# Performance work log

Hardware: AMD Instinct MI355X
Metric: run time of the kernel (lower is better)

## Reference

```python
import jax, jax.numpy as jnp
import numpy as np

DEPTH = 4      # truncation depth of the signature
DIM = 8        # path channels
PATH_LEN = 16384
STREAM = True


def _restricted_exp(z, depth):
    # exp(z) in truncated tensor algebra: level k term = z^{\otimes k}/k!, flattened to [d**k]
    terms = [z]
    for k in range(2, depth + 1):
        terms.append((terms[-1][:, None] * z[None, :]).reshape(-1) / k)
    return tuple(terms)


def _chen_mult(a, b, depth):
    # Truncated tensor-algebra product (Chen's relation); a_0 = b_0 = 1 implicit.
    # c_k = a_k + b_k + sum_{i=1}^{k-1} a_i \otimes b_{k-i}
    c = []
    for k in range(depth):
        t = a[k] + b[k]
        for i in range(k):
            t = t + (a[i][:, None] * b[k - 1 - i][None, :]).reshape(-1)
        c.append(t)
    return tuple(c)


def setup_inputs() -> dict:
    key = jax.random.key(0)
    path = jax.random.normal(key, (PATH_LEN, DIM), dtype=jnp.float32)
    return {"path": path}


def reference(path):
    depth = DEPTH
    d = path.shape[-1]
    inc = path[1:] - path[:-1]                                # [N-1, d] increments
    exps = jax.vmap(lambda z: _restricted_exp(z, depth))(inc)  # tuple of [N-1, d**k]
    init = tuple(jnp.zeros((d ** (k + 1),), dtype=path.dtype) for k in range(depth))

    def step(carry, x):
        new = _chen_mult(carry, x, depth)
        return new, (new if STREAM else None)

    last, ys = jax.lax.scan(step, init, exps)
    if STREAM:
        # flatten: concat levels -> [N-1, d + d^2 + ... + d^depth]
        return jnp.concatenate([y for y in ys], axis=-1)
    return jnp.concatenate(last, axis=-1)
```

## Files before the change

### kernel.cpp

```cpp
#include <hip/hip_runtime.h>

#define NPATH 16384
#define DIM   8
#define NINC  (NPATH - 1)
#define SIG   4680
#define L1OFF 0
#define L2OFF 8
#define L3OFF 72
#define L4OFF 584
#define NBLK  256
#define CHUNK 64
#define NGRP  16
#define GSIZE 16
#define C6    0.16666666666666666f


__device__ __forceinline__ void store_sig_reg(float* __restrict__ dst,
                                              const float r4[16], const float r3[2],
                                              float a2s, float a1t, int t) {
  float4* d4 = (float4*)(dst + L4OFF + 16 * t);
  d4[0] = make_float4(r4[0], r4[1], r4[2], r4[3]);
  d4[1] = make_float4(r4[4], r4[5], r4[6], r4[7]);
  d4[2] = make_float4(r4[8], r4[9], r4[10], r4[11]);
  d4[3] = make_float4(r4[12], r4[13], r4[14], r4[15]);
  *(float2*)(dst + L3OFF + 2 * t) = make_float2(r3[0], r3[1]);
  if (t < 64) dst[L2OFF + t] = a2s;
  if (t < 8)  dst[L1OFF + t] = a1t;
}

__device__ __forceinline__ void chen_reg(float r4[16], float r3[2],
                                         float& a1i, float& a2v,
                                         float& a2s, float& a1s, float& a1t,
                                         const float* __restrict__ b, int t) {
  const int i   = t >> 5;
  const int j   = (t >> 2) & 7;
  const int ij  = t >> 2;
  const int c0  = 2 * t;
  const int jk0 = c0 & 63;
  const int k0  = 2 * (t & 3);
  const int i2  = t >> 3;
  const int j2  = t & 7;
  const float4* bv = (const float4*)b;
  float4 B0 = bv[146 + 4 * t], B1 = bv[147 + 4 * t], B2 = bv[148 + 4 * t], B3 = bv[149 + 4 * t];
  float4 Cq0 = bv[18 + 2 * jk0], Cq1 = bv[19 + 2 * jk0], Cq2 = bv[20 + 2 * jk0], Cq3 = bv[21 + 2 * jk0];
  float4 D0 = bv[2 + 2 * k0], D1 = bv[3 + 2 * k0], D2 = bv[4 + 2 * k0], D3 = bv[5 + 2 * k0];
  float4 E0 = bv[0], E1 = bv[1];
  const float2 b3c  = *(const float2*)(b + L3OFF + c0);
  const float2 b2jk = *(const float2*)(b + L2OFF + jk0);
  const float2 b1k  = *(const float2*)(b + L1OFF + k0);
  const float b2ij = b[L2OFF + ij];
  const float b1j  = b[L1OFF + j];
  const float b1i  = b[L1OFF + i];
  float b2t = 0.f, b1j2 = 0.f, b1i2 = 0.f, b1t = 0.f;
  if (t < 64) { b2t = b[L2OFF + t]; b1j2 = b[L1OFF + j2]; b1i2 = b[L1OFF + i2]; }
  if (t < 8)  { b1t = b[L1OFF + t]; }

  const float b4r[16] = {B0.x,B0.y,B0.z,B0.w, B1.x,B1.y,B1.z,B1.w,
                         B2.x,B2.y,B2.z,B2.w, B3.x,B3.y,B3.z,B3.w};
  const float b3r[16] = {Cq0.x,Cq0.y,Cq0.z,Cq0.w, Cq1.x,Cq1.y,Cq1.z,Cq1.w,
                         Cq2.x,Cq2.y,Cq2.z,Cq2.w, Cq3.x,Cq3.y,Cq3.z,Cq3.w};
  const float b2r[16] = {D0.x,D0.y,D0.z,D0.w, D1.x,D1.y,D1.z,D1.w,
                         D2.x,D2.y,D2.z,D2.w, D3.x,D3.y,D3.z,D3.w};
  const float b1r[8]  = {E0.x,E0.y,E0.z,E0.w, E1.x,E1.y,E1.z,E1.w};

#pragma unroll
  for (int l = 0; l < 8; ++l) {
    r4[l]     += b4r[l]     + a1i * b3r[l]     + a2v * b2r[l]     + r3[0] * b1r[l];
    r4[8 + l] += b4r[8 + l] + a1i * b3r[8 + l] + a2v * b2r[8 + l] + r3[1] * b1r[l];
  }
  r3[0] += b3c.x + a1i * b2jk.x + a2v * b1k.x;
  r3[1] += b3c.y + a1i * b2jk.y + a2v * b1k.y;
  const float a1i_old = a1i;
  a2v += b2ij + a1i_old * b1j;
  if (t < 64) { a2s += b2t + a1s * b1j2; a1s += b1i2; }
  a1i = a1i_old + b1i;
  if (t < 8) a1t += b1t;
}

__device__ __forceinline__ void fill_zbuf(float (*zbuf)[8], const float* __restrict__ path,
                                          int base, int t) {
  for (int u = t; u < CHUNK * 8; u += 256) {
    const int s = u >> 3, l = u & 7;
    const int rB = min(base + s + 1, NPATH - 1);
    zbuf[s][l] = path[rB * DIM + l] - path[(base + s) * DIM + l];
  }
}

template <bool STORE>
__device__ __forceinline__ void run_steps(const float (*zbuf)[8],
                                          float* __restrict__ out, int base, int nsteps,
                                          float r4[16], float r3[2],
                                          float& a1i, float& a2v,
                                          float& a2s, float& a1s, float& a1t, int t) {
  const int i  = t >> 5;
  const int j  = (t >> 2) & 7;
  const int k0 = 2 * (t & 3);
  const int i2 = t >> 3;
  const int j2 = t & 7;
  for (int s = 0; s < nsteps; ++s) {
    const float* zs = zbuf[s];
    const float zi = zs[i];
    const float zj = zs[j];
    const float2 zk = *(const float2*)(zs + k0);
    const float4 za = *(const float4*)zs;
    const float4 zb = *(const float4*)(zs + 4);
    const float zn[8] = {za.x, za.y, za.z, za.w, zb.x, zb.y, zb.z, zb.w};
    const float a1zi4 = a1i + 0.25f * zi;
    const float zj6   = C6 * zj;
    const float T0 = r3[0] + a2v * (0.5f * zk.x) + a1zi4 * (zj6 * zk.x);
    const float T1 = r3[1] + a2v * (0.5f * zk.y) + a1zi4 * (zj6 * zk.y);
    const float U  = a2v + (0.5f * a1i + C6 * zi) * zj;
#pragma unroll
    for (int l = 0; l < 8; ++l) {
      r4[l]     += T0 * zn[l];
      r4[8 + l] += T1 * zn[l];
    }
    r3[0] += zk.x * U;
    r3[1] += zk.y * U;
    a2v += (a1i + 0.5f * zi) * zj;
    a1i += zi;
    if (t < 64) {
      const float zi2 = zs[i2], zj2v = zs[j2];
      a2s += (a1s + 0.5f * zi2) * zj2v;
      a1s += zi2;
    }
    if (t < 8) a1t += zs[t];
    if constexpr (STORE) {
      float* dst = out + (size_t)(base + s) * SIG;
      float4* d4 = (float4*)(dst + L4OFF + 16 * t);
      d4[0] = make_float4(r4[0], r4[1], r4[2], r4[3]);
      d4[1] = make_float4(r4[4], r4[5], r4[6], r4[7]);
      d4[2] = make_float4(r4[8], r4[9], r4[10], r4[11]);
      d4[3] = make_float4(r4[12], r4[13], r4[14], r4[15]);
      *(float2*)(dst + L3OFF + 2 * t) = make_float2(r3[0], r3[1]);
      if (t < 64) dst[L2OFF + t] = a2s;
      if (t < 8)  dst[L1OFF + t] = a1t;
    }
  }
}

__global__ __launch_bounds__(256) void k_chunk_totals(const float* __restrict__ path,
                                                      float* __restrict__ totals) {
  __shared__ float zbuf[CHUNK][8];
  const int t = threadIdx.x;
  const int b = blockIdx.x;
  const int base = b * CHUNK;
  const int n = min(CHUNK, NINC - base);
  fill_zbuf(zbuf, path, base, t);
  float r4[16];
#pragma unroll
  for (int l = 0; l < 16; ++l) r4[l] = 0.f;
  float r3[2] = {0.f, 0.f};
  float a1i = 0.f, a2v = 0.f, a2s = 0.f, a1s = 0.f, a1t = 0.f;
  __syncthreads();
  run_steps<false>(zbuf, nullptr, base, n, r4, r3, a1i, a2v, a2s, a1s, a1t, t);
  store_sig_reg(totals + (size_t)b * SIG, r4, r3, a2s, a1t, t);
}

__global__ __launch_bounds__(256) void k_scan(const float* __restrict__ in,
                                              float* __restrict__ prefout,
                                              float* __restrict__ totout,
                                              int count) {
  const int t = threadIdx.x;
  const size_t goff = (size_t)blockIdx.x * count;
  float r4[16];
#pragma unroll
  for (int l = 0; l < 16; ++l) r4[l] = 0.f;
  float r3[2] = {0.f, 0.f};
  float a1i = 0.f, a2v = 0.f, a2s = 0.f, a1s = 0.f, a1t = 0.f;
  for (int m = 0; m < count; ++m) {
    store_sig_reg(prefout + (goff + m) * SIG, r4, r3, a2s, a1t, t);
    chen_reg(r4, r3, a1i, a2v, a2s, a1s, a1t, in + (goff + m) * SIG, t);
  }
  if (totout != nullptr) store_sig_reg(totout + (size_t)blockIdx.x * SIG, r4, r3, a2s, a1t, t);
}

__global__ __launch_bounds__(256) void k_phase3(const float* __restrict__ path,
                                                const float* __restrict__ pref,
                                                const float* __restrict__ gpref,
                                                float* __restrict__ out) {
  __shared__ float zbuf[CHUNK][8];
  const int t = threadIdx.x;
  const int b = blockIdx.x;
  const int g = b >> 4;
  const int base = b * CHUNK;
  const int n = min(CHUNK, NINC - base);
  fill_zbuf(zbuf, path, base, t);
  const float* gp = gpref + (size_t)g * SIG;
  const float4* g4 = (const float4*)(gp + L4OFF + 16 * t);
  float4 G0 = g4[0], G1 = g4[1], G2 = g4[2], G3 = g4[3];
  float r4[16] = {G0.x,G0.y,G0.z,G0.w, G1.x,G1.y,G1.z,G1.w,
                  G2.x,G2.y,G2.z,G2.w, G3.x,G3.y,G3.z,G3.w};
  const float2 gr3 = *(const float2*)(gp + L3OFF + 2 * t);
  float r3[2] = {gr3.x, gr3.y};
  float a1i = gp[L1OFF + (t >> 5)];
  float a2v = gp[L2OFF + (t >> 2)];
  float a2s = 0.f, a1s = 0.f, a1t = 0.f;
  if (t < 64) { a2s = gp[L2OFF + t]; a1s = gp[L1OFF + (t >> 3)]; }
  if (t < 8)  { a1t = gp[L1OFF + t]; }
  chen_reg(r4, r3, a1i, a2v, a2s, a1s, a1t, pref + (size_t)b * SIG, t);
  __syncthreads();
  run_steps<true>(zbuf, out, base, n, r4, r3, a1i, a2v, a2s, a1s, a1t, t);
}

extern "C" void kernel_launch(void* const* d_in, const int* in_sizes, int n_in,
                              void* d_out, int out_size, void* d_ws, size_t ws_size,
                              hipStream_t stream) {
  (void)in_sizes; (void)n_in; (void)out_size; (void)ws_size;
  const float* path = (const float*)d_in[0];
  float* out = (float*)d_out;
  float* ws = (float*)d_ws;

  float* totals = ws;
  float* pref   = totals + (size_t)NBLK * SIG;
  float* gtot   = pref   + (size_t)NBLK * SIG;
  float* gpref  = gtot   + (size_t)NGRP * SIG;

  k_chunk_totals<<<NBLK, 256, 0, stream>>>(path, totals);
  k_scan<<<NGRP, 256, 0, stream>>>(totals, pref, gtot, GSIZE);
  k_scan<<<1, 256, 0, stream>>>(gtot, gpref, nullptr, NGRP);
  k_phase3<<<NBLK, 256, 0, stream>>>(path, pref, gpref, out);
}
```

Measured before the change: 153.9 us.

## Fuse four-kernel signature scan into one cooperative kernel with grid syncs

Merges the chunk-totals, two scan passes and final streaming pass into a single cooperative kernel that uses grid-wide syncs in place of separate launches. Each block builds its own exclusive prefix by redundantly Chen-multiplying the preceding totals within its group, then the preceding group totals. Level-4 output stores are staged through a padded, double-buffered LDS buffer so each wavefront writes contiguous memory. This removes launch gaps and the serial single-block scan, at the cost of redundant prefix work per block, a per-step barrier and cooperative-launch constraints.

After: 193.5 us. 1.26x slower.

```diff
diff --git a/kernel.cpp b/kernel.cpp
--- a/kernel.cpp
+++ b/kernel.cpp
@@ -1,4 +1,7 @@
 #include <hip/hip_runtime.h>
+#include <hip/hip_cooperative_groups.h>
+
+namespace cg = cooperative_groups;
 
 #define NPATH 16384
 #define DIM   8
@@ -10,12 +13,26 @@
 #define L4OFF 584
 #define NBLK  256
 #define CHUNK 64
-#define NGRP  16
 #define GSIZE 16
 #define C6    0.16666666666666666f
-
-
-__device__ __forceinline__ void store_sig_reg(float* __restrict__ dst,
+#define LPAD  17
+
+
+__device__ __forceinline__ void light_barrier() {
+  asm volatile("s_waitcnt lgkmcnt(0)" ::: "memory");
+  __builtin_amdgcn_s_barrier();
+}
+
+__device__ __forceinline__ void zero_state(float r4[16], float r3[2],
+                                           float& a1i, float& a2v,
+                                           float& a2s, float& a1s, float& a1t) {
+#pragma unroll
+  for (int l = 0; l < 16; ++l) r4[l] = 0.f;
+  r3[0] = r3[1] = 0.f;
+  a1i = a2v = a2s = a1s = a1t = 0.f;
+}
+
+__device__ __forceinline__ void store_sig_reg(float* dst,
                                               const float r4[16], const float r3[2],
                                               float a2s, float a1t, int t) {
   float4* d4 = (float4*)(dst + L4OFF + 16 * t);
@@ -31,7 +48,7 @@
 __device__ __forceinline__ void chen_reg(float r4[16], float r3[2],
                                          float& a1i, float& a2v,
                                          float& a2s, float& a1s, float& a1t,
-                                         const float* __restrict__ b, int t) {
+                                         const float* b, int t) {
   const int i   = t >> 5;
   const int j   = (t >> 2) & 7;
   const int ij  = t >> 2;
@@ -87,7 +104,7 @@
 }
 
 template <bool STORE>
-__device__ __forceinline__ void run_steps(const float (*zbuf)[8],
+__device__ __forceinline__ void run_steps(const float (*zbuf)[8], float* lbuf,
                                           float* __restrict__ out, int base, int nsteps,
                                           float r4[16], float r3[2],
                                           float& a1i, float& a2v,
@@ -97,6 +114,8 @@
   const int k0 = 2 * (t & 3);
   const int i2 = t >> 3;
   const int j2 = t & 7;
+  const int tp = t >> 2;
+  const int rq = 4 * (t & 3);
   for (int s = 0; s < nsteps; ++s) {
     const float* zs = zbuf[s];
     const float zi = zs[i];
@@ -126,12 +145,19 @@
     }
     if (t < 8) a1t += zs[t];
     if constexpr (STORE) {
+      float* lb = lbuf + (s & 1) * (256 * LPAD) + LPAD * t;
+      *(float4*)(lb + 0)  = make_float4(r4[0], r4[1], r4[2], r4[3]);
+      *(float4*)(lb + 4)  = make_float4(r4[4], r4[5], r4[6], r4[7]);
+      *(float4*)(lb + 8)  = make_float4(r4[8], r4[9], r4[10], r4[11]);
+      *(float4*)(lb + 12) = make_float4(r4[12], r4[13], r4[14], r4[15]);
+      light_barrier();
+      const float* lbr = lbuf + (s & 1) * (256 * LPAD);
       float* dst = out + (size_t)(base + s) * SIG;
-      float4* d4 = (float4*)(dst + L4OFF + 16 * t);
-      d4[0] = make_float4(r4[0], r4[1], r4[2], r4[3]);
-      d4[1] = make_float4(r4[4], r4[5], r4[6], r4[7]);
-      d4[2] = make_float4(r4[8], r4[9], r4[10], r4[11]);
-      d4[3] = make_float4(r4[12], r4[13], r4[14], r4[15]);
+#pragma unroll
+      for (int q = 0; q < 4; ++q) {
+        const float4 v = *(const float4*)(lbr + LPAD * (tp + 64 * q) + rq);
+        *(float4*)(dst + L4OFF + 4 * t + 1024 * q) = v;
+      }
       *(float2*)(dst + L3OFF + 2 * t) = make_float2(r3[0], r3[1]);
       if (t < 64) dst[L2OFF + t] = a2s;
       if (t < 8)  dst[L1OFF + t] = a1t;
@@ -139,68 +165,51 @@
   }
 }
 
-__global__ __launch_bounds__(256) void k_chunk_totals(const float* __restrict__ path,
-                                                      float* __restrict__ totals) {
+__global__ __launch_bounds__(256) void k_fused(const float* __restrict__ path,
+                                               float* __restrict__ ws,
+                                               float* __restrict__ out) {
   __shared__ float zbuf[CHUNK][8];
-  const int t = threadIdx.x;
-  const int b = blockIdx.x;
-  const int base = b * CHUNK;
-  const int n = min(CHUNK, NINC - base);
-  fill_zbuf(zbuf, path, base, t);
-  float r4[16];
-#pragma unroll
-  for (int l = 0; l < 16; ++l) r4[l] = 0.f;
-  float r3[2] = {0.f, 0.f};
-  float a1i = 0.f, a2v = 0.f, a2s = 0.f, a1s = 0.f, a1t = 0.f;
-  __syncthreads();
-  run_steps<false>(zbuf, nullptr, base, n, r4, r3, a1i, a2v, a2s, a1s, a1t, t);
-  store_sig_reg(totals + (size_t)b * SIG, r4, r3, a2s, a1t, t);
-}
-
-__global__ __launch_bounds__(256) void k_scan(const float* __restrict__ in,
-                                              float* __restrict__ prefout,
-                                              float* __restrict__ totout,
-                                              int count) {
-  const int t = threadIdx.x;
-  const size_t goff = (size_t)blockIdx.x * count;
-  float r4[16];
-#pragma unroll
-  for (int l = 0; l < 16; ++l) r4[l] = 0.f;
-  float r3[2] = {0.f, 0.f};
-  float a1i = 0.f, a2v = 0.f, a2s = 0.f, a1s = 0.f, a1t = 0.f;
-  for (int m = 0; m < count; ++m) {
-    store_sig_reg(prefout + (goff + m) * SIG, r4, r3, a2s, a1t, t);
-    chen_reg(r4, r3, a1i, a2v, a2s, a1s, a1t, in + (goff + m) * SIG, t);
-  }
-  if (totout != nullptr) store_sig_reg(totout + (size_t)blockIdx.x * SIG, r4, r3, a2s, a1t, t);
-}
-
-__global__ __launch_bounds__(256) void k_phase3(const float* __restrict__ path,
-                                                const float* __restrict__ pref,
-                                                const float* __restrict__ gpref,
-                                                float* __restrict__ out) {
-  __shared__ float zbuf[CHUNK][8];
+  __shared__ __align__(16) float ldsE[SIG];
+  __shared__ __align__(16) float lbuf[2 * 256 * LPAD];
   const int t = threadIdx.x;
   const int b = blockIdx.x;
   const int g = b >> 4;
   const int base = b * CHUNK;
   const int n = min(CHUNK, NINC - base);
+  float* totals = ws;
+  float* GT     = ws + (size_t)NBLK * SIG;
+
   fill_zbuf(zbuf, path, base, t);
-  const float* gp = gpref + (size_t)g * SIG;
-  const float4* g4 = (const float4*)(gp + L4OFF + 16 * t);
-  float4 G0 = g4[0], G1 = g4[1], G2 = g4[2], G3 = g4[3];
-  float r4[16] = {G0.x,G0.y,G0.z,G0.w, G1.x,G1.y,G1.z,G1.w,
-                  G2.x,G2.y,G2.z,G2.w, G3.x,G3.y,G3.z,G3.w};
-  const float2 gr3 = *(const float2*)(gp + L3OFF + 2 * t);
-  float r3[2] = {gr3.x, gr3.y};
-  float a1i = gp[L1OFF + (t >> 5)];
-  float a2v = gp[L2OFF + (t >> 2)];
-  float a2s = 0.f, a1s = 0.f, a1t = 0.f;
-  if (t < 64) { a2s = gp[L2OFF + t]; a1s = gp[L1OFF + (t >> 3)]; }
-  if (t < 8)  { a1t = gp[L1OFF + t]; }
-  chen_reg(r4, r3, a1i, a2v, a2s, a1s, a1t, pref + (size_t)b * SIG, t);
+  float r4[16], r3[2], a1i, a2v, a2s, a1s, a1t;
+  zero_state(r4, r3, a1i, a2v, a2s, a1s, a1t);
   __syncthreads();
-  run_steps<true>(zbuf, out, base, n, r4, r3, a1i, a2v, a2s, a1s, a1t, t);
+  run_steps<false>(zbuf, nullptr, nullptr, base, n, r4, r3, a1i, a2v, a2s, a1s, a1t, t);
+  store_sig_reg(totals + (size_t)b * SIG, r4, r3, a2s, a1t, t);
+
+  cg::this_grid().sync();
+
+  zero_state(r4, r3, a1i, a2v, a2s, a1s, a1t);
+  for (int m = g * GSIZE; m < b; ++m)
+    chen_reg(r4, r3, a1i, a2v, a2s, a1s, a1t, totals + (size_t)m * SIG, t);
+  if ((b & (GSIZE - 1)) == (GSIZE - 1)) {
+    float c4[16], c3[2];
+#pragma unroll
+    for (int l = 0; l < 16; ++l) c4[l] = r4[l];
+    c3[0] = r3[0]; c3[1] = r3[1];
+    float c1i = a1i, c2v = a2v, c2s = a2s, c1s = a1s, c1t = a1t;
+    chen_reg(c4, c3, c1i, c2v, c2s, c1s, c1t, totals + (size_t)b * SIG, t);
+    store_sig_reg(GT + (size_t)g * SIG, c4, c3, c2s, c1t, t);
+  }
+  store_sig_reg(ldsE, r4, r3, a2s, a1t, t);
+
+  cg::this_grid().sync();
+
+  zero_state(r4, r3, a1i, a2v, a2s, a1s, a1t);
+  for (int gp = 0; gp < g; ++gp)
+    chen_reg(r4, r3, a1i, a2v, a2s, a1s, a1t, GT + (size_t)gp * SIG, t);
+  chen_reg(r4, r3, a1i, a2v, a2s, a1s, a1t, ldsE, t);
+
+  run_steps<true>(zbuf, lbuf, out, base, n, r4, r3, a1i, a2v, a2s, a1s, a1t, t);
 }
 
 extern "C" void kernel_launch(void* const* d_in, const int* in_sizes, int n_in,
@@ -210,14 +219,6 @@
   const float* path = (const float*)d_in[0];
   float* out = (float*)d_out;
   float* ws = (float*)d_ws;
-
-  float* totals = ws;
-  float* pref   = totals + (size_t)NBLK * SIG;
-  float* gtot   = pref   + (size_t)NBLK * SIG;
-  float* gpref  = gtot   + (size_t)NGRP * SIG;
-
-  k_chunk_totals<<<NBLK, 256, 0, stream>>>(path, totals);
-  k_scan<<<NGRP, 256, 0, stream>>>(totals, pref, gtot, GSIZE);
-  k_scan<<<1, 256, 0, stream>>>(gtot, gpref, nullptr, NGRP);
-  k_phase3<<<NBLK, 256, 0, stream>>>(path, pref, gpref, out);
-}
+  void* args[] = {(void*)&path, (void*)&ws, (void*)&out};
+  hipLaunchCooperativeKernel((const void*)k_fused, dim3(NBLK), dim3(256), args, 0, stream);
+}
```
